# Kernel tuning notes

Measured on AMD Instinct MI355X. Metric: run time of the kernel, lower is better.

## Reference

```python
import jax, jax.numpy as jnp
import numpy as np

B, T, D, V, E = 128, 256, 1024, 32000, 300


def setup_inputs() -> dict:
    key = jax.random.key(0)
    ks = jax.random.split(key, 9)
    s = lambda d: 1.0 / np.sqrt(d)
    return {
        "input_to_decoder": jax.random.randint(ks[0], (B, 1), 0, V),
        "encoder_output": jax.random.normal(ks[1], (B, T, D), jnp.float32) * s(D),
        "state_h": jax.random.normal(ks[2], (B, D), jnp.float32) * s(D),
        "state_c": jax.random.normal(ks[3], (B, D), jnp.float32) * s(D),
        "emb_table": jax.random.normal(ks[4], (V, E), jnp.float32) * 0.02,
        "W_lstm": jax.random.normal(ks[5], (D + E, 4 * D), jnp.float32) * s(D + E),
        "U_lstm": jax.random.normal(ks[6], (D, 4 * D), jnp.float32) * s(D),
        "b_lstm": jnp.zeros((4 * D,), jnp.float32),
        "W_dense": jax.random.normal(ks[7], (D, V), jnp.float32) * s(D),
        "b_dense": jnp.zeros((V,), jnp.float32),
    }


def reference(input_to_decoder, encoder_output, state_h, state_c,
              emb_table, W_lstm, U_lstm, b_lstm, W_dense, b_dense):
    # embedding lookup + squeeze(axis=1): [B,1] -> [B,E]
    emb = emb_table[input_to_decoder[:, 0]]
    # Bahdanau-style dot scores: [B,T]
    scores = jnp.einsum("btd,bd->bt", encoder_output, state_h)
    # NOTE: faithful to source - context uses RAW (pre-softmax) scores
    context = jnp.einsum("btd,bt->bd", encoder_output, scores)  # [B,D]
    attention_weights = jax.nn.softmax(scores, axis=1)[..., None]  # [B,T,1]
    # concat context + embedding, single LSTM cell step (Keras gate order i,f,g,o)
    x = jnp.concatenate([context, emb], axis=1)  # [B,D+E]
    z = x @ W_lstm + state_h @ U_lstm + b_lstm  # [B,4D]
    zi, zf, zg, zo = jnp.split(z, 4, axis=1)
    c_new = jax.nn.sigmoid(zf) * state_c + jax.nn.sigmoid(zi) * jnp.tanh(zg)
    h_new = jax.nn.sigmoid(zo) * jnp.tanh(c_new)
    logits = h_new @ W_dense + b_dense  # [B,V]
    return logits, h_new, c_new, attention_weights, context
```

## Files before the change

kernel.cpp:

```cpp
#include <hip/hip_runtime.h>
#include <hip/hip_bf16.h>
#include <cmath>


#define Bc 128
#define Tc 256
#define Dc 1024
#define Vc 32000
#define Ec 300
#define KREAL 2348
#define KXP 2688
#define KSPLIT 7
#define N4 4096

typedef __attribute__((ext_vector_type(8))) short bf16x8;
typedef __attribute__((ext_vector_type(4))) float f32x4;

static __device__ __forceinline__ short f2bf(float x) {
    __hip_bfloat16 b = __float2bfloat16(x);
    return *reinterpret_cast<short*>(&b);
}
static __device__ __forceinline__ unsigned pack2(float a, float b) {
    return (unsigned)(unsigned short)f2bf(a) | ((unsigned)(unsigned short)f2bf(b) << 16);
}

__global__ void k_att1(const float* __restrict__ enc, const float* __restrict__ h,
                       float* __restrict__ scores_g, float* __restrict__ ctx_part) {
    const int tc = blockIdx.x;
    const int b  = blockIdx.y;
    const int tid = threadIdx.x;
    const int wave = tid >> 6, lane = tid & 63;
    __shared__ float s_lds[32];

    const float4* h4 = (const float4*)(h + ((size_t)b << 10));
    float4 hv0 = h4[lane], hv1 = h4[lane + 64], hv2 = h4[lane + 128], hv3 = h4[lane + 192];

    #pragma unroll 2
    for (int i = 0; i < 8; ++i) {
        int tl = (wave << 3) + i;
        int t  = (tc << 5) + tl;
        const float4* e4 = (const float4*)(enc + ((size_t)(b * Tc + t) << 10));
        float4 e0 = e4[lane], e1 = e4[lane + 64], e2 = e4[lane + 128], e3 = e4[lane + 192];
        float d = e0.x*hv0.x + e0.y*hv0.y + e0.z*hv0.z + e0.w*hv0.w
                + e1.x*hv1.x + e1.y*hv1.y + e1.z*hv1.z + e1.w*hv1.w
                + e2.x*hv2.x + e2.y*hv2.y + e2.z*hv2.z + e2.w*hv2.w
                + e3.x*hv3.x + e3.y*hv3.y + e3.z*hv3.z + e3.w*hv3.w;
        #pragma unroll
        for (int off = 32; off; off >>= 1) d += __shfl_xor(d, off, 64);
        if (lane == 0) { s_lds[tl] = d; scores_g[(b << 8) + t] = d; }
    }
    __syncthreads();

    const float* ep = enc + ((size_t)(b * Tc + (tc << 5)) << 10) + (tid << 2);
    float4 acc = {0.f, 0.f, 0.f, 0.f};
    #pragma unroll 8
    for (int tl = 0; tl < 32; ++tl) {
        float4 v = *(const float4*)(ep + ((size_t)tl << 10));
        float s = s_lds[tl];
        acc.x += s * v.x; acc.y += s * v.y; acc.z += s * v.z; acc.w += s * v.w;
    }
    *(float4*)(ctx_part + (((size_t)(tc << 7) + b) << 10) + (tid << 2)) = acc;
}

__global__ void k_att2(const float* __restrict__ ctx_part, const float* __restrict__ scores_g,
                       const int* __restrict__ idx, const float* __restrict__ emb_table,
                       const float* __restrict__ h,
                       float* __restrict__ ctx_out, float* __restrict__ attn_out,
                       unsigned short* __restrict__ x_bf) {
    const int b = blockIdx.x;
    const int tid = threadIdx.x;
    __shared__ float red[256];

    float4 cv = {0.f, 0.f, 0.f, 0.f};
    #pragma unroll
    for (int tc = 0; tc < 8; ++tc) {
        float4 s = *(const float4*)(ctx_part + (((size_t)(tc << 7) + b) << 10) + (tid << 2));
        cv.x += s.x; cv.y += s.y; cv.z += s.z; cv.w += s.w;
    }
    *(float4*)(ctx_out + ((size_t)b << 10) + (tid << 2)) = cv;

    unsigned short* xb = x_bf + (size_t)b * KXP;
    uint2 p0; p0.x = pack2(cv.x, cv.y); p0.y = pack2(cv.z, cv.w);
    *(uint2*)&xb[tid << 2] = p0;

    int row = idx[b];
    for (int i = tid; i < Ec; i += 256)
        xb[Dc + i] = (unsigned short)f2bf(emb_table[(size_t)row * Ec + i]);

    float4 hv = *(const float4*)(h + ((size_t)b << 10) + (tid << 2));
    uint2 p1; p1.x = pack2(hv.x, hv.y); p1.y = pack2(hv.z, hv.w);
    *(uint2*)&xb[(Dc + Ec) + (tid << 2)] = p1;

    for (int i = tid; i < KXP - KREAL; i += 256) xb[KREAL + i] = 0;

    float v = scores_g[(b << 8) + tid];
    red[tid] = v;
    __syncthreads();
    for (int s = 128; s; s >>= 1) { if (tid < s) red[tid] = fmaxf(red[tid], red[tid + s]); __syncthreads(); }
    float m = red[0];
    __syncthreads();
    float e = __expf(v - m);
    red[tid] = e;
    __syncthreads();
    for (int s = 128; s; s >>= 1) { if (tid < s) red[tid] += red[tid + s]; __syncthreads(); }
    attn_out[(b << 8) + tid] = e / red[0];
}

__global__ __launch_bounds__(512) void k_zgemm_mfma(
        const unsigned short* __restrict__ xbf, const float* __restrict__ Wl,
        const float* __restrict__ Ul, float* __restrict__ z_part) {
    __shared__ __align__(16) short blds[2 * 8 * 64 * 8];
    const int tid  = threadIdx.x;
    const int wid  = tid >> 6;
    const int lane = tid & 63;
    const int g    = lane >> 4;
    const int r    = lane & 15;
    const int n0   = blockIdx.x << 6;
    const int ksp  = blockIdx.y;

    const int pr = tid >> 4;
    const int c  = tid & 15;
    const int kk = (pr << 1) & 31;
    const int gg = kk >> 3, jj = kk & 7;
    const int ks0 = pr >> 4;

    f32x4 acc[4] = {};
    const unsigned short* xrow = xbf + (size_t)((wid << 4) + r) * KXP;

    float4 wra[2], wrb[2];
    bf16x8 areg[2][2];

    auto loadWU = [&](int gk) -> float4 {
        if (gk < 1324) return *(const float4*)(Wl + (size_t)gk * N4 + n0 + (c << 2));
        if (gk < KREAL) return *(const float4*)(Ul + (size_t)(gk - 1324) * N4 + n0 + (c << 2));
        return float4{0.f, 0.f, 0.f, 0.f};
    };

    {
        const int kt = (ksp * 6) << 6;
        wra[0] = loadWU(kt + (pr << 1));
        wrb[0] = loadWU(kt + (pr << 1) + 1);
        areg[0][0] = *(const bf16x8*)&xrow[kt + (g << 3)];
        areg[0][1] = *(const bf16x8*)&xrow[kt + 32 + (g << 3)];
    }

    #pragma unroll
    for (int t = 0; t < 6; ++t) {
        const int cur = t & 1;
        const int coff = cur << 12;
        {
            const float av[4] = {wra[cur].x, wra[cur].y, wra[cur].z, wra[cur].w};
            const float bv[4] = {wrb[cur].x, wrb[cur].y, wrb[cur].z, wrb[cur].w};
            #pragma unroll
            for (int i = 0; i < 4; ++i) {
                int n = (c << 2) + i;
                int nt = n >> 4;
                int inner = (gg << 4) | (n & 15);
                int Xs = ((((ks0 << 2) + nt) << 6) | inner) ^ nt;
                *(unsigned*)&blds[coff + (Xs << 3) + jj] = pack2(av[i], bv[i]);
            }
        }
        if (t < 5) {
            const int kt = ((ksp * 6) + t + 1) << 6;
            wra[cur ^ 1] = loadWU(kt + (pr << 1));
            wrb[cur ^ 1] = loadWU(kt + (pr << 1) + 1);
            areg[cur ^ 1][0] = *(const bf16x8*)&xrow[kt + (g << 3)];
            areg[cur ^ 1][1] = *(const bf16x8*)&xrow[kt + 32 + (g << 3)];
        }
        __syncthreads();
        #pragma unroll
        for (int ks = 0; ks < 2; ++ks) {
            #pragma unroll
            for (int nt = 0; nt < 4; ++nt) {
                int Xs = ((((ks << 2) + nt) << 6) | lane) ^ nt;
                bf16x8 bfr = *(const bf16x8*)&blds[coff + (Xs << 3)];
                acc[nt] = __builtin_amdgcn_mfma_f32_16x16x32_bf16(areg[cur][ks], bfr, acc[nt], 0, 0, 0);
            }
        }
    }

    float* zp = z_part + ((size_t)ksp << 19);
    #pragma unroll
    for (int nt = 0; nt < 4; ++nt) {
        int col = n0 + (nt << 4) + r;
        #pragma unroll
        for (int j = 0; j < 4; ++j) {
            int rowm = (wid << 4) + (g << 2) + j;
            zp[((size_t)rowm << 12) + col] = acc[nt][j];
        }
    }
}

__global__ void k_gates(const float* __restrict__ z_part, const float* __restrict__ b_lstm,
                        const float* __restrict__ c_in, float* __restrict__ h_new,
                        float* __restrict__ c_new, unsigned short* __restrict__ h_bf) {
    int i = blockIdx.x * 256 + threadIdx.x;
    int b = i >> 10, d = i & 1023;
    size_t base = ((size_t)b << 12) + d;
    float zi = b_lstm[d], zf = b_lstm[d + 1024], zg = b_lstm[d + 2048], zo = b_lstm[d + 3072];
    #pragma unroll
    for (int ks = 0; ks < KSPLIT; ++ks) {
        const float* zp = z_part + ((size_t)ks << 19);
        zi += zp[base];
        zf += zp[base + 1024];
        zg += zp[base + 2048];
        zo += zp[base + 3072];
    }
    float si = 1.f / (1.f + __expf(-zi));
    float sf = 1.f / (1.f + __expf(-zf));
    float so = 1.f / (1.f + __expf(-zo));
    float cn = sf * c_in[i] + si * tanhf(zg);
    float hn = so * tanhf(cn);
    c_new[i] = cn;
    h_new[i] = hn;
    h_bf[i] = (unsigned short)f2bf(hn);
}

__global__ __launch_bounds__(512) void k_logits_mfma(
        const unsigned short* __restrict__ hbf, const float* __restrict__ Wd,
        const float* __restrict__ bd, float* __restrict__ out) {
    __shared__ __align__(16) short blds[2 * 16 * 64 * 8];
    const int tid  = threadIdx.x;
    const int wid  = tid >> 6;
    const int lane = tid & 63;
    const int g    = lane >> 4;
    const int r    = lane & 15;
    const int n0   = blockIdx.x << 6;

    const int pr = tid >> 4;
    const int c  = tid & 15;
    const int kk = (pr << 1) & 31;
    const int gg = kk >> 3, jj = kk & 7;
    const int ksA = pr >> 4;
    const int ksB = ksA + 2;

    f32x4 acc[4] = {};
    const unsigned short* hrow = hbf + ((size_t)((wid << 4) + r) << 10);
    const float* wbase = Wd + (size_t)(pr << 1) * Vc + n0 + (c << 2);

    float4 wra[2], wrb[2], wrc[2], wrd[2];
    bf16x8 areg[2][4];

    {
        wra[0] = *(const float4*)(wbase);
        wrb[0] = *(const float4*)(wbase + Vc);
        wrc[0] = *(const float4*)(wbase + (size_t)64 * Vc);
        wrd[0] = *(const float4*)(wbase + (size_t)65 * Vc);
        #pragma unroll
        for (int ks = 0; ks < 4; ++ks)
            areg[0][ks] = *(const bf16x8*)&hrow[(ks << 5) + (g << 3)];
    }

    #pragma unroll
    for (int t = 0; t < 8; ++t) {
        const int cur = t & 1;
        const int coff = cur << 13;
        {
            const float a0[4] = {wra[cur].x, wra[cur].y, wra[cur].z, wra[cur].w};
            const float b0[4] = {wrb[cur].x, wrb[cur].y, wrb[cur].z, wrb[cur].w};
            const float c0[4] = {wrc[cur].x, wrc[cur].y, wrc[cur].z, wrc[cur].w};
            const float d0[4] = {wrd[cur].x, wrd[cur].y, wrd[cur].z, wrd[cur].w};
            #pragma unroll
            for (int i = 0; i < 4; ++i) {
                int n = (c << 2) + i;
                int nt = n >> 4;
                int inner = (gg << 4) | (n & 15);
                int XsA = ((((ksA << 2) + nt) << 6) | inner) ^ nt;
                int XsB = ((((ksB << 2) + nt) << 6) | inner) ^ nt;
                *(unsigned*)&blds[coff + (XsA << 3) + jj] = pack2(a0[i], b0[i]);
                *(unsigned*)&blds[coff + (XsB << 3) + jj] = pack2(c0[i], d0[i]);
            }
        }
        if (t < 7) {
            const float* wb2 = wbase + (size_t)((t + 1) << 7) * Vc;
            wra[cur ^ 1] = *(const float4*)(wb2);
            wrb[cur ^ 1] = *(const float4*)(wb2 + Vc);
            wrc[cur ^ 1] = *(const float4*)(wb2 + (size_t)64 * Vc);
            wrd[cur ^ 1] = *(const float4*)(wb2 + (size_t)65 * Vc);
            #pragma unroll
            for (int ks = 0; ks < 4; ++ks)
                areg[cur ^ 1][ks] = *(const bf16x8*)&hrow[((t + 1) << 7) + (ks << 5) + (g << 3)];
        }
        __syncthreads();
        #pragma unroll
        for (int ks = 0; ks < 4; ++ks) {
            #pragma unroll
            for (int nt = 0; nt < 4; ++nt) {
                int Xs = ((((ks << 2) + nt) << 6) | lane) ^ nt;
                bf16x8 bfr = *(const bf16x8*)&blds[coff + (Xs << 3)];
                acc[nt] = __builtin_amdgcn_mfma_f32_16x16x32_bf16(areg[cur][ks], bfr, acc[nt], 0, 0, 0);
            }
        }
    }

    #pragma unroll
    for (int nt = 0; nt < 4; ++nt) {
        int col = n0 + (nt << 4) + r;
        float bias = bd[col];
        #pragma unroll
        for (int j = 0; j < 4; ++j) {
            int row = (wid << 4) + (g << 2) + j;
            out[(size_t)row * Vc + col] = acc[nt][j] + bias;
        }
    }
}

extern "C" void kernel_launch(void* const* d_in, const int* in_sizes, int n_in,
                              void* d_out, int out_size, void* d_ws, size_t ws_size,
                              hipStream_t stream) {
    const int*   idx = (const int*)d_in[0];
    const float* enc = (const float*)d_in[1];
    const float* h   = (const float*)d_in[2];
    const float* c   = (const float*)d_in[3];
    const float* emb = (const float*)d_in[4];
    const float* Wl  = (const float*)d_in[5];
    const float* Ul  = (const float*)d_in[6];
    const float* bl  = (const float*)d_in[7];
    const float* Wd  = (const float*)d_in[8];
    const float* bd  = (const float*)d_in[9];

    float* out    = (float*)d_out;
    float* logits = out;
    float* h_new  = out + 4096000;
    float* c_new  = out + 4227072;
    float* attn   = out + 4358144;
    float* ctx    = out + 4390912;

    float*          ctx_part = out;
    float*          scores_g = out + 1048576;
    float*          z_part   = out;
    unsigned short* x_bf16   = (unsigned short*)d_ws;
    unsigned short* h_bf16   = (unsigned short*)d_ws + 344064;

    hipLaunchKernelGGL(k_att1, dim3(8, 128), dim3(256), 0, stream, enc, h, scores_g, ctx_part);
    hipLaunchKernelGGL(k_att2, dim3(128), dim3(256), 0, stream, ctx_part, scores_g, idx, emb, h,
                       ctx, attn, x_bf16);
    hipLaunchKernelGGL(k_zgemm_mfma, dim3(64, KSPLIT), dim3(512), 0, stream, x_bf16, Wl, Ul, z_part);
    hipLaunchKernelGGL(k_gates, dim3(512), dim3(256), 0, stream, z_part, bl, c, h_new, c_new, h_bf16);
    hipLaunchKernelGGL(k_logits_mfma, dim3(500), dim3(512), 0, stream, h_bf16, Wd, bd, logits);
}
```

Baseline: 104.7 us.

## Fuse attention score and context accumulation into one pass over encoder rows

The attention kernel now accumulates the context contribution in registers while it computes each score, so each encoder row is read once instead of twice. Per-wave partial contexts are reduced through LDS. Each block now covers 64 time steps instead of 32, which halves the grid, the partial-context buffer and the reduction work in the second kernel. The cost is more registers per thread, 16KB of LDS per block and fewer blocks to hide the memory traffic of the large encoder tensor.

```diff
diff --git a/kernel.cpp b/kernel.cpp
--- a/kernel.cpp
+++ b/kernel.cpp
@@ -30,36 +30,47 @@
     const int b  = blockIdx.y;
     const int tid = threadIdx.x;
     const int wave = tid >> 6, lane = tid & 63;
-    __shared__ float s_lds[32];
+    __shared__ float s_acc[4][1024];
 
     const float4* h4 = (const float4*)(h + ((size_t)b << 10));
     float4 hv0 = h4[lane], hv1 = h4[lane + 64], hv2 = h4[lane + 128], hv3 = h4[lane + 192];
 
+    float4 a0 = {0,0,0,0}, a1 = {0,0,0,0}, a2 = {0,0,0,0}, a3 = {0,0,0,0};
+    const int t0 = (tc << 6) + (wave << 4);
+    const float4* e4 = (const float4*)(enc + ((size_t)(b * Tc + t0) << 10));
+
     #pragma unroll 2
-    for (int i = 0; i < 8; ++i) {
-        int tl = (wave << 3) + i;
-        int t  = (tc << 5) + tl;
-        const float4* e4 = (const float4*)(enc + ((size_t)(b * Tc + t) << 10));
+    for (int i = 0; i < 16; ++i) {
         float4 e0 = e4[lane], e1 = e4[lane + 64], e2 = e4[lane + 128], e3 = e4[lane + 192];
+        e4 += 256;
         float d = e0.x*hv0.x + e0.y*hv0.y + e0.z*hv0.z + e0.w*hv0.w
                 + e1.x*hv1.x + e1.y*hv1.y + e1.z*hv1.z + e1.w*hv1.w
                 + e2.x*hv2.x + e2.y*hv2.y + e2.z*hv2.z + e2.w*hv2.w
                 + e3.x*hv3.x + e3.y*hv3.y + e3.z*hv3.z + e3.w*hv3.w;
         #pragma unroll
         for (int off = 32; off; off >>= 1) d += __shfl_xor(d, off, 64);
-        if (lane == 0) { s_lds[tl] = d; scores_g[(b << 8) + t] = d; }
-    }
+        if (lane == 0) scores_g[(b << 8) + t0 + i] = d;
+        a0.x += d*e0.x; a0.y += d*e0.y; a0.z += d*e0.z; a0.w += d*e0.w;
+        a1.x += d*e1.x; a1.y += d*e1.y; a1.z += d*e1.z; a1.w += d*e1.w;
+        a2.x += d*e2.x; a2.y += d*e2.y; a2.z += d*e2.z; a2.w += d*e2.w;
+        a3.x += d*e3.x; a3.y += d*e3.y; a3.z += d*e3.z; a3.w += d*e3.w;
+    }
+
+    *(float4*)&s_acc[wave][lane << 2]         = a0;
+    *(float4*)&s_acc[wave][256 + (lane << 2)] = a1;
+    *(float4*)&s_acc[wave][512 + (lane << 2)] = a2;
+    *(float4*)&s_acc[wave][768 + (lane << 2)] = a3;
     __syncthreads();
-
-    const float* ep = enc + ((size_t)(b * Tc + (tc << 5)) << 10) + (tid << 2);
-    float4 acc = {0.f, 0.f, 0.f, 0.f};
-    #pragma unroll 8
-    for (int tl = 0; tl < 32; ++tl) {
-        float4 v = *(const float4*)(ep + ((size_t)tl << 10));
-        float s = s_lds[tl];
-        acc.x += s * v.x; acc.y += s * v.y; acc.z += s * v.z; acc.w += s * v.w;
-    }
-    *(float4*)(ctx_part + (((size_t)(tc << 7) + b) << 10) + (tid << 2)) = acc;
+    float4 r0 = *(const float4*)&s_acc[0][tid << 2];
+    float4 r1 = *(const float4*)&s_acc[1][tid << 2];
+    float4 r2 = *(const float4*)&s_acc[2][tid << 2];
+    float4 r3 = *(const float4*)&s_acc[3][tid << 2];
+    float4 r;
+    r.x = r0.x + r1.x + r2.x + r3.x;
+    r.y = r0.y + r1.y + r2.y + r3.y;
+    r.z = r0.z + r1.z + r2.z + r3.z;
+    r.w = r0.w + r1.w + r2.w + r3.w;
+    *(float4*)(ctx_part + (((size_t)(tc << 7) + b) << 10) + (tid << 2)) = r;
 }
 
 __global__ void k_att2(const float* __restrict__ ctx_part, const float* __restrict__ scores_g,
@@ -73,7 +84,7 @@
 
     float4 cv = {0.f, 0.f, 0.f, 0.f};
     #pragma unroll
-    for (int tc = 0; tc < 8; ++tc) {
+    for (int tc = 0; tc < 4; ++tc) {
         float4 s = *(const float4*)(ctx_part + (((size_t)(tc << 7) + b) << 10) + (tid << 2));
         cv.x += s.x; cv.y += s.y; cv.z += s.z; cv.w += s.w;
     }
@@ -327,12 +338,12 @@
     float* ctx    = out + 4390912;
 
     float*          ctx_part = out;
-    float*          scores_g = out + 1048576;
+    float*          scores_g = out + 524288;
     float*          z_part   = out;
     unsigned short* x_bf16   = (unsigned short*)d_ws;
     unsigned short* h_bf16   = (unsigned short*)d_ws + 344064;
 
-    hipLaunchKernelGGL(k_att1, dim3(8, 128), dim3(256), 0, stream, enc, h, scores_g, ctx_part);
+    hipLaunchKernelGGL(k_att1, dim3(4, 128), dim3(256), 0, stream, enc, h, scores_g, ctx_part);
     hipLaunchKernelGGL(k_att2, dim3(128), dim3(256), 0, stream, ctx_part, scores_g, idx, emb, h,
                        ctx, attn, x_bf16);
     hipLaunchKernelGGL(k_zgemm_mfma, dim3(64, KSPLIT), dim3(512), 0, stream, x_bf16, Wl, Ul, z_part);
```

Result: faster. 91.15 us (median of 2 runs) (-13.0%).
